# Optimization experiments

Measured on AMD Instinct MI355X. Metric: run time of the kernel, lower is better.

## Reference

```python
import jax, jax.numpy as jnp
import numpy as np
from itertools import product

G = 96          # voxel grid side
B = 2           # batch samples
N_PER = 60000   # occupied voxels per sample
N = B * N_PER
C_IN = 64
C_OUT = 1
NUM_BLOCKS = 2
EPS = 1e-5


def _build_kernel_map():
    """Emulate MinkowskiEngine's coordinate hash map for a k=3, stride=1, 3D conv.
    Returns batch_ids [N], and per-offset (in_idx, out_idx) padded to N with sentinel N."""
    rng = np.random.default_rng(0)
    side = G - 2  # coords in [1, G-2] so offset coords never wrap
    keys_list = []
    for b in range(B):
        lin = rng.choice(side ** 3, size=N_PER, replace=False)
        x = lin // (side * side) + 1
        y = (lin // side) % side + 1
        z = lin % side + 1
        keys_list.append(b * G ** 3 + x * G * G + y * G + z)
    keys = np.concatenate(keys_list)
    batch_ids = np.repeat(np.arange(B), N_PER).astype(np.int32)
    order = np.argsort(keys)
    skeys = keys[order]
    in_idx = np.full((27, N), N, np.int32)   # sentinel N -> zero-padded feature row
    out_idx = np.full((27, N), N, np.int32)  # sentinel N -> dropped output row
    for k, (dx, dy, dz) in enumerate(product((-1, 0, 1), repeat=3)):
        nk = keys + dx * G * G + dy * G + dz  # neighbor coordinate key per output voxel
        pos = np.searchsorted(skeys, nk)
        pc = np.clip(pos, 0, N - 1)
        valid = skeys[pc] == nk
        m = int(valid.sum())
        in_idx[k, :m] = order[pc[valid]]
        out_idx[k, :m] = np.nonzero(valid)[0]
    return batch_ids, in_idx, out_idx


def instance_norm(f, batch_ids, num_batches):
    # per-sample, per-channel normalization over all voxels of each sample (ME InstanceNorm, no affine)
    cnt = jax.ops.segment_sum(jnp.ones((f.shape[0],), f.dtype), batch_ids, num_segments=num_batches)
    mean = jax.ops.segment_sum(f, batch_ids, num_segments=num_batches) / cnt[:, None]
    fc = f - mean[batch_ids]
    var = jax.ops.segment_sum(fc * fc, batch_ids, num_segments=num_batches) / cnt[:, None]
    return fc * jax.lax.rsqrt(var + EPS)[batch_ids]


def sparse_conv(f, w, in_idx, out_idx, bias=None):
    # gather-matmul-scatter per kernel offset; w: [27, Cin, Cout]
    n = f.shape[0]
    fpad = jnp.concatenate([f, jnp.zeros((1, f.shape[1]), f.dtype)], axis=0)
    out = jnp.zeros((n + 1, w.shape[-1]), f.dtype)
    for k in range(w.shape[0]):  # static 27-iteration loop over kernel offsets
        out = out.at[out_idx[k]].add(fpad[in_idx[k]] @ w[k])
    out = out[:n]
    if bias is not None:
        out = out + bias
    return out


def setup_inputs() -> dict:
    batch_ids, in_idx, out_idx = _build_kernel_map()
    key = jax.random.key(0)
    k0, k1, k2, k3 = jax.random.split(key, 4)
    feats = jax.random.normal(k0, (N, C_IN), dtype=jnp.float32)
    w_blocks = jax.random.normal(k1, (NUM_BLOCKS, 2, 27, C_IN, C_IN), dtype=jnp.float32) * 0.02
    w_final = jax.random.normal(k2, (27, C_IN, C_OUT), dtype=jnp.float32) * 0.02
    b_final = jax.random.normal(k3, (C_OUT,), dtype=jnp.float32) * 0.02
    return {
        "feats": feats,
        "w_blocks": w_blocks,
        "w_final": w_final,
        "b_final": b_final,
        "in_idx": jnp.asarray(in_idx),
        "out_idx": jnp.asarray(out_idx),
        "batch_ids": jnp.asarray(batch_ids),
        "batch_size": B,
    }


def reference(feats, w_blocks, w_final, b_final, in_idx, out_idx, batch_ids, batch_size):
    # InstanceNorm + ReLU
    x = jax.nn.relu(instance_norm(feats, batch_ids, batch_size))
    # SparseBasicBlocks: conv -> IN -> relu -> conv -> IN -> +res -> relu
    for b in range(w_blocks.shape[0]):
        res = x
        h = sparse_conv(x, w_blocks[b, 0], in_idx, out_idx)
        h = jax.nn.relu(instance_norm(h, batch_ids, batch_size))
        h = sparse_conv(h, w_blocks[b, 1], in_idx, out_idx)
        h = instance_norm(h, batch_ids, batch_size)
        x = jax.nn.relu(h + res)
    # final conv with bias
    return sparse_conv(x, w_final, in_idx, out_idx, bias=b_final)
```

## Files before the change

### kernel.cpp

```cpp
#include <hip/hip_runtime.h>

#define NPTS 120000
#define NROW 120064
#define NB   60000
#define TAPS 27
#define NBLK (NROW / 128)

typedef short  short8 __attribute__((ext_vector_type(8)));
typedef float  f32x4  __attribute__((ext_vector_type(4)));

__device__ __forceinline__ float bf2f(unsigned short u) {
  unsigned v = ((unsigned)u) << 16;
  float f; __builtin_memcpy(&f, &v, 4); return f;
}
__device__ __forceinline__ unsigned short f2bf(float f) {
  unsigned v; __builtin_memcpy(&v, &f, 4);
  v = v + 0x7FFFu + ((v >> 16) & 1u);
  return (unsigned short)(v >> 16);
}

__global__ __launch_bounds__(256) void k_build_nbr(const int* __restrict__ oi,
                                                   const int* __restrict__ ii,
                                                   int* __restrict__ nbr) {
  int g = blockIdx.x * 256 + threadIdx.x;
  if (g >= TAPS * NPTS) return;
  int o = oi[g];
  if (o < NPTS) nbr[(g / NPTS) * NROW + o] = ii[g];
}

__global__ __launch_bounds__(256) void k_repack(const float* __restrict__ w,
                                                unsigned short* __restrict__ wp) {
  int g = blockIdx.x * 256 + threadIdx.x;
  int e = g & 7, l = (g >> 3) & 63, f = (g >> 9) & 7, rest = g >> 12;
  int t = f >> 1, h = f & 1;
  int kk = h * 32 + (l >> 4) * 8 + e;
  int cc = t * 16 + (l & 15);
  wp[g] = f2bf(w[(rest * 64 + kk) * 64 + cc]);
}

__global__ __launch_bounds__(256) void k_stats1_f32(const float* __restrict__ F,
                                                    float* __restrict__ SM) {
  int lane = threadIdx.x & 63, wave = threadIdx.x >> 6;
  int batch = blockIdx.x >> 7, bb = blockIdx.x & 127;
  const float* Fb = F + (size_t)batch * NB * 64;
  float s = 0.f, ss = 0.f;
  for (int r = bb * 4 + wave; r < NB; r += 512) {
    float v = Fb[(size_t)r * 64 + lane];
    s += v; ss += v * v;
  }
  __shared__ float ls[4][64], lss[4][64];
  ls[wave][lane] = s; lss[wave][lane] = ss;
  __syncthreads();
  if (threadIdx.x < 64) {
    float S  = ls[0][lane] + ls[1][lane] + ls[2][lane] + ls[3][lane];
    float SS = lss[0][lane] + lss[1][lane] + lss[2][lane] + lss[3][lane];
    atomicAdd(&SM[(batch * 2 + 0) * 64 + lane], S);
    atomicAdd(&SM[(batch * 2 + 1) * 64 + lane], SS);
  }
}

__global__ __launch_bounds__(256) void k_apply_f2b(const float* __restrict__ F,
                                                   const float* __restrict__ SM,
                                                   unsigned short* __restrict__ O) {
  int i = blockIdx.x * 256 + threadIdx.x;
  int r = i >> 3, cb = (i & 7) * 8;
  int b = (r >= NB) ? 1 : 0;
  f32x4 v0 = *((const f32x4*)F + i * 2);
  f32x4 v1 = *((const f32x4*)F + i * 2 + 1);
  short8 o;
#pragma unroll
  for (int e = 0; e < 8; ++e) {
    float mean = SM[(b * 2 + 0) * 64 + cb + e] * (1.f / NB);
    float var  = SM[(b * 2 + 1) * 64 + cb + e] * (1.f / NB) - mean * mean;
    float rstd = rsqrtf(var + 1e-5f);
    float x = (e < 4) ? v0[e & 3] : v1[e & 3];
    o[e] = (short)f2bf(fmaxf((x - mean) * rstd, 0.f));
  }
  *((short8*)O + i) = o;
}

__global__ __launch_bounds__(256) void k_apply_bf(const unsigned short* __restrict__ F,
                                                  const float* __restrict__ SM,
                                                  unsigned short* __restrict__ O) {
  int i = blockIdx.x * 256 + threadIdx.x;
  int r = i >> 3, cb = (i & 7) * 8;
  int b = (r >= NB) ? 1 : 0;
  short8 v = *((const short8*)F + i);
  short8 o;
#pragma unroll
  for (int e = 0; e < 8; ++e) {
    float mean = SM[(b * 2 + 0) * 64 + cb + e] * (1.f / NB);
    float var  = SM[(b * 2 + 1) * 64 + cb + e] * (1.f / NB) - mean * mean;
    float rstd = rsqrtf(var + 1e-5f);
    float f = (bf2f((unsigned short)v[e]) - mean) * rstd;
    o[e] = (short)f2bf(fmaxf(f, 0.f));
  }
  *((short8*)O + i) = o;
}

__global__ __launch_bounds__(256) void k_apply_res_bf(const unsigned short* __restrict__ H2,
                                                      const float* __restrict__ SM,
                                                      unsigned short* __restrict__ X) {
  int i = blockIdx.x * 256 + threadIdx.x;
  int r = i >> 3, cb = (i & 7) * 8;
  int b = (r >= NB) ? 1 : 0;
  short8 v = *((const short8*)H2 + i);
  short8 xv = *((const short8*)X + i);
  short8 o;
#pragma unroll
  for (int e = 0; e < 8; ++e) {
    float mean = SM[(b * 2 + 0) * 64 + cb + e] * (1.f / NB);
    float var  = SM[(b * 2 + 1) * 64 + cb + e] * (1.f / NB) - mean * mean;
    float rstd = rsqrtf(var + 1e-5f);
    float f = (bf2f((unsigned short)v[e]) - mean) * rstd + bf2f((unsigned short)xv[e]);
    o[e] = (short)f2bf(fmaxf(f, 0.f));
  }
  *((short8*)X + i) = o;
}

__global__ __launch_bounds__(256) void k_conv64s(const unsigned short* __restrict__ X,
                                                 const unsigned short* __restrict__ WP,
                                                 const int* __restrict__ nbr,
                                                 unsigned short* __restrict__ Y,
                                                 float* __restrict__ SM) {
  const int lane = threadIdx.x & 63, wave = threadIdx.x >> 6;
  const int j0w = blockIdx.x * 128 + wave * 32;
  const int lrow = lane & 15, lk = lane >> 4;
  const int nb0 = j0w + lrow;
  f32x4 acc[2][4];
#pragma unroll
  for (int g = 0; g < 2; ++g)
#pragma unroll
    for (int c = 0; c < 4; ++c) acc[g][c] = (f32x4){0.f, 0.f, 0.f, 0.f};

  short8 aA[2][2], aB[2][2];

  auto GATHER = [&](int k, short8 (&a)[2][2]) {
    const int* np = nbr + (size_t)k * NROW + nb0;
    int i0 = np[0], i1 = np[16];
    const unsigned short* r0 = X + (size_t)(i0 >= 0 ? i0 : NROW) * 64 + lk * 8;
    const unsigned short* r1 = X + (size_t)(i1 >= 0 ? i1 : NROW) * 64 + lk * 8;
    a[0][0] = *(const short8*)r0; a[0][1] = *(const short8*)(r0 + 32);
    a[1][0] = *(const short8*)r1; a[1][1] = *(const short8*)(r1 + 32);
  };
  auto TAP = [&](int k, short8 (&a)[2][2]) {
    const unsigned short* wpk = WP + k * 4096 + lane * 8;
#pragma unroll
    for (int ct = 0; ct < 4; ++ct) {
      short8 b0 = *(const short8*)(wpk + ct * 1024);
      short8 b1 = *(const short8*)(wpk + ct * 1024 + 512);
      acc[0][ct] = __builtin_amdgcn_mfma_f32_16x16x32_bf16(a[0][0], b0, acc[0][ct], 0, 0, 0);
      acc[0][ct] = __builtin_amdgcn_mfma_f32_16x16x32_bf16(a[0][1], b1, acc[0][ct], 0, 0, 0);
      acc[1][ct] = __builtin_amdgcn_mfma_f32_16x16x32_bf16(a[1][0], b0, acc[1][ct], 0, 0, 0);
      acc[1][ct] = __builtin_amdgcn_mfma_f32_16x16x32_bf16(a[1][1], b1, acc[1][ct], 0, 0, 0);
    }
  };

  GATHER(0, aA);
#pragma unroll
  for (int kk = 0; kk < TAPS; kk += 2) {
    if (kk + 1 < TAPS) GATHER(kk + 1, aB);
    TAP(kk, aA);
    if (kk + 1 < TAPS) {
      if (kk + 2 < TAPS) GATHER(kk + 2, aA);
      TAP(kk + 1, aB);
    }
  }

#pragma unroll
  for (int g = 0; g < 2; ++g) {
    unsigned short* yp = Y + (size_t)(j0w + g * 16 + lk * 4) * 64 + lrow;
#pragma unroll
    for (int r = 0; r < 4; ++r) {
      yp[r * 64 +  0] = f2bf(acc[g][0][r]);
      yp[r * 64 + 16] = f2bf(acc[g][1][r]);
      yp[r * 64 + 32] = f2bf(acc[g][2][r]);
      yp[r * 64 + 48] = f2bf(acc[g][3][r]);
    }
  }

  float s[4][2], q[4][2];
#pragma unroll
  for (int ct = 0; ct < 4; ++ct) { s[ct][0] = s[ct][1] = q[ct][0] = q[ct][1] = 0.f; }
#pragma unroll
  for (int g = 0; g < 2; ++g) {
    int rowbase = j0w + g * 16 + lk * 4;
#pragma unroll
    for (int r = 0; r < 4; ++r) {
      int bt = (rowbase + r) >= NB;
#pragma unroll
      for (int ct = 0; ct < 4; ++ct) {
        float v = acc[g][ct][r];
        s[ct][bt] += v; q[ct][bt] += v * v;
      }
    }
  }
  __shared__ float sred[4][4][4][64];
#pragma unroll
  for (int ct = 0; ct < 4; ++ct)
#pragma unroll
    for (int b = 0; b < 2; ++b) {
      sred[wave][lk][b * 2 + 0][ct * 16 + lrow] = s[ct][b];
      sred[wave][lk][b * 2 + 1][ct * 16 + lrow] = q[ct][b];
    }
  __syncthreads();
  int t = threadIdx.x;
  float S = 0.f;
#pragma unroll
  for (int w = 0; w < 4; ++w)
#pragma unroll
    for (int l2 = 0; l2 < 4; ++l2)
      S += sred[w][l2][t >> 6][t & 63];
  atomicAdd(&SM[t], S);
}

__global__ __launch_bounds__(256) void k_dfin(const unsigned short* __restrict__ X,
                                              const float* __restrict__ WF,
                                              float* __restrict__ D) {
  const int lane = threadIdx.x & 63, wave = threadIdx.x >> 6;
  const int j0 = blockIdx.x * 64 + wave * 16;
  const int lrow = lane & 15, lk = lane >> 4;
  const unsigned short* rp = X + (size_t)(j0 + lrow) * 64 + lk * 8;
  short8 a0 = *(const short8*)rp;
  short8 a1 = *(const short8*)(rp + 32);
  short8 b[2][2];
#pragma unroll
  for (int ct = 0; ct < 2; ++ct) {
    int col = ct * 16 + lrow;
#pragma unroll
    for (int h = 0; h < 2; ++h) {
#pragma unroll
      for (int e = 0; e < 8; ++e)
        b[ct][h][e] = (col < TAPS) ? (short)f2bf(WF[col * 64 + h * 32 + lk * 8 + e]) : (short)0;
    }
  }
  f32x4 acc0 = {0,0,0,0}, acc1 = {0,0,0,0};
  acc0 = __builtin_amdgcn_mfma_f32_16x16x32_bf16(a0, b[0][0], acc0, 0, 0, 0);
  acc0 = __builtin_amdgcn_mfma_f32_16x16x32_bf16(a1, b[0][1], acc0, 0, 0, 0);
  acc1 = __builtin_amdgcn_mfma_f32_16x16x32_bf16(a0, b[1][0], acc1, 0, 0, 0);
  acc1 = __builtin_amdgcn_mfma_f32_16x16x32_bf16(a1, b[1][1], acc1, 0, 0, 0);
  float* dp0 = D + (size_t)lrow * NROW + j0 + lk * 4;
  float* dp1 = D + (size_t)(16 + lrow) * NROW + j0 + lk * 4;
#pragma unroll
  for (int r = 0; r < 4; ++r) { dp0[r] = acc0[r]; dp1[r] = acc1[r]; }
}

__global__ __launch_bounds__(256) void k_gfin(const float* __restrict__ D,
                                              const int* __restrict__ nbr,
                                              const float* __restrict__ BF,
                                              float* __restrict__ out) {
  int j = blockIdx.x * 256 + threadIdx.x;
  if (j >= NPTS) return;
  float acc = BF[0];
#pragma unroll
  for (int k = 0; k < TAPS; ++k) {
    int idx = nbr[(size_t)k * NROW + j];
    if (idx >= 0) acc += D[(size_t)k * NROW + idx];
  }
  out[j] = acc;
}

extern "C" void kernel_launch(void* const* d_in, const int* in_sizes, int n_in,
                              void* d_out, int out_size, void* d_ws, size_t ws_size,
                              hipStream_t stream) {
  (void)in_sizes; (void)n_in; (void)out_size; (void)ws_size;
  const float* feats = (const float*)d_in[0];
  const float* wblk  = (const float*)d_in[1];
  const float* wfin  = (const float*)d_in[2];
  const float* bfin  = (const float*)d_in[3];
  const int* in_idx  = (const int*)d_in[4];
  const int* out_idx = (const int*)d_in[5];

  char* p = (char*)d_ws;
  size_t off = 0;
  auto carve = [&](size_t bytes) {
    void* r = p + off; off += (bytes + 255) & ~(size_t)255; return r;
  };
  int*            nbr = (int*)carve((size_t)TAPS * NROW * 4);
  unsigned short* Xb  = (unsigned short*)carve((size_t)(NROW + 1) * 64 * 2);
  unsigned short* Hb  = (unsigned short*)carve((size_t)(NROW + 1) * 64 * 2);
  unsigned short* H2b = (unsigned short*)carve((size_t)NROW * 64 * 2);
  unsigned short* WP  = (unsigned short*)carve(108u * 4096u * 2);
  float*          D   = (float*)carve((size_t)32 * NROW * 4);
  float*          SMa = (float*)carve(5 * 256 * 4);

  float* SM0 = SMa;
  float* SM1 = SMa + 256;
  float* SM2 = SMa + 512;
  float* SM3 = SMa + 768;
  float* SM4 = SMa + 1024;

  hipMemsetAsync(nbr, 0xFF, (size_t)TAPS * NROW * 4, stream);
  hipMemsetAsync(SMa, 0, 5 * 256 * 4, stream);
  hipMemsetAsync(Xb + (size_t)NROW * 64, 0, 128, stream);
  hipMemsetAsync(Hb + (size_t)NROW * 64, 0, 128, stream);
  k_build_nbr<<<(TAPS * NPTS + 255) / 256, 256, 0, stream>>>(out_idx, in_idx, nbr);
  k_repack<<<1728, 256, 0, stream>>>(wblk, WP);

  k_stats1_f32<<<256, 256, 0, stream>>>(feats, SM0);
  k_apply_f2b<<<3750, 256, 0, stream>>>(feats, SM0, Xb);

  k_conv64s<<<NBLK, 256, 0, stream>>>(Xb, WP + 0 * 110592, nbr, Hb, SM1);
  k_apply_bf<<<3750, 256, 0, stream>>>(Hb, SM1, Hb);
  k_conv64s<<<NBLK, 256, 0, stream>>>(Hb, WP + 1 * 110592, nbr, H2b, SM2);
  k_apply_res_bf<<<3750, 256, 0, stream>>>(H2b, SM2, Xb);

  k_conv64s<<<NBLK, 256, 0, stream>>>(Xb, WP + 2 * 110592, nbr, Hb, SM3);
  k_apply_bf<<<3750, 256, 0, stream>>>(Hb, SM3, Hb);
  k_conv64s<<<NBLK, 256, 0, stream>>>(Hb, WP + 3 * 110592, nbr, H2b, SM4);
  k_apply_res_bf<<<3750, 256, 0, stream>>>(H2b, SM4, Xb);

  k_dfin<<<NROW / 64, 256, 0, stream>>>(Xb, wfin, D);
  k_gfin<<<NROW / 256, 256, 0, stream>>>(D, nbr, bfin, (float*)d_out);
}
```

Measured before the change: 451.4 us.

## Stage conv weights in LDS with double-buffered async loads and skip empty taps

The sparse conv kernel now copies each tap's 64x64 bf16 weight slice into a double-buffered LDS area using global_load_lds, prefetching the next tap while the current one is computed. Every wave then reads weights from LDS instead of each wave reading them from global memory. Taps where no row in the wave has a valid neighbor skip the gather and the MFMAs, decided by a wave ballot. In exchange the explicit register double-buffering of gathered rows is gone, a block-wide barrier is added on every tap, and the loop is no longer unrolled, so gather latency may be hidden less well.

```diff
diff --git a/kernel.cpp b/kernel.cpp
--- a/kernel.cpp
+++ b/kernel.cpp
@@ -8,6 +8,9 @@
 
 typedef short  short8 __attribute__((ext_vector_type(8)));
 typedef float  f32x4  __attribute__((ext_vector_type(4)));
+typedef unsigned int u32;
+#define GLB __attribute__((address_space(1)))
+#define LDS __attribute__((address_space(3)))
 
 __device__ __forceinline__ float bf2f(unsigned short u) {
   unsigned v = ((unsigned)u) << 16;
@@ -124,47 +127,57 @@
                                                  unsigned short* __restrict__ Y,
                                                  float* __restrict__ SM) {
   const int lane = threadIdx.x & 63, wave = threadIdx.x >> 6;
+  const int t = threadIdx.x;
   const int j0w = blockIdx.x * 128 + wave * 32;
   const int lrow = lane & 15, lk = lane >> 4;
   const int nb0 = j0w + lrow;
+
+  __shared__ unsigned short wbuf[2][4096];
+  __shared__ float sred[4][4][4][64];
+
+  {
+    const unsigned short* g = WP;
+    __builtin_amdgcn_global_load_lds((GLB const u32*)(g + t * 8),
+                                     (LDS u32*)&wbuf[0][t * 8], 16, 0, 0);
+    __builtin_amdgcn_global_load_lds((GLB const u32*)(g + (t + 256) * 8),
+                                     (LDS u32*)&wbuf[0][(t + 256) * 8], 16, 0, 0);
+  }
+  __syncthreads();
+
   f32x4 acc[2][4];
 #pragma unroll
   for (int g = 0; g < 2; ++g)
 #pragma unroll
     for (int c = 0; c < 4; ++c) acc[g][c] = (f32x4){0.f, 0.f, 0.f, 0.f};
 
-  short8 aA[2][2], aB[2][2];
-
-  auto GATHER = [&](int k, short8 (&a)[2][2]) {
+  for (int k = 0; k < TAPS; ++k) {
+    const int cur = k & 1;
+    if (k + 1 < TAPS) {
+      const unsigned short* g = WP + (k + 1) * 4096;
+      __builtin_amdgcn_global_load_lds((GLB const u32*)(g + t * 8),
+                                       (LDS u32*)&wbuf[cur ^ 1][t * 8], 16, 0, 0);
+      __builtin_amdgcn_global_load_lds((GLB const u32*)(g + (t + 256) * 8),
+                                       (LDS u32*)&wbuf[cur ^ 1][(t + 256) * 8], 16, 0, 0);
+    }
     const int* np = nbr + (size_t)k * NROW + nb0;
     int i0 = np[0], i1 = np[16];
-    const unsigned short* r0 = X + (size_t)(i0 >= 0 ? i0 : NROW) * 64 + lk * 8;
-    const unsigned short* r1 = X + (size_t)(i1 >= 0 ? i1 : NROW) * 64 + lk * 8;
-    a[0][0] = *(const short8*)r0; a[0][1] = *(const short8*)(r0 + 32);
-    a[1][0] = *(const short8*)r1; a[1][1] = *(const short8*)(r1 + 32);
-  };
-  auto TAP = [&](int k, short8 (&a)[2][2]) {
-    const unsigned short* wpk = WP + k * 4096 + lane * 8;
-#pragma unroll
-    for (int ct = 0; ct < 4; ++ct) {
-      short8 b0 = *(const short8*)(wpk + ct * 1024);
-      short8 b1 = *(const short8*)(wpk + ct * 1024 + 512);
-      acc[0][ct] = __builtin_amdgcn_mfma_f32_16x16x32_bf16(a[0][0], b0, acc[0][ct], 0, 0, 0);
-      acc[0][ct] = __builtin_amdgcn_mfma_f32_16x16x32_bf16(a[0][1], b1, acc[0][ct], 0, 0, 0);
-      acc[1][ct] = __builtin_amdgcn_mfma_f32_16x16x32_bf16(a[1][0], b0, acc[1][ct], 0, 0, 0);
-      acc[1][ct] = __builtin_amdgcn_mfma_f32_16x16x32_bf16(a[1][1], b1, acc[1][ct], 0, 0, 0);
-    }
-  };
-
-  GATHER(0, aA);
-#pragma unroll
-  for (int kk = 0; kk < TAPS; kk += 2) {
-    if (kk + 1 < TAPS) GATHER(kk + 1, aB);
-    TAP(kk, aA);
-    if (kk + 1 < TAPS) {
-      if (kk + 2 < TAPS) GATHER(kk + 2, aA);
-      TAP(kk + 1, aB);
-    }
+    if (__ballot(i0 >= 0 || i1 >= 0) != 0ull) {
+      const unsigned short* r0 = X + (size_t)(i0 >= 0 ? i0 : NROW) * 64 + lk * 8;
+      const unsigned short* r1 = X + (size_t)(i1 >= 0 ? i1 : NROW) * 64 + lk * 8;
+      short8 a00 = *(const short8*)r0, a01 = *(const short8*)(r0 + 32);
+      short8 a10 = *(const short8*)r1, a11 = *(const short8*)(r1 + 32);
+      const unsigned short* wl = &wbuf[cur][lane * 8];
+#pragma unroll
+      for (int ct = 0; ct < 4; ++ct) {
+        short8 b0 = *(const short8*)(wl + ct * 1024);
+        short8 b1 = *(const short8*)(wl + ct * 1024 + 512);
+        acc[0][ct] = __builtin_amdgcn_mfma_f32_16x16x32_bf16(a00, b0, acc[0][ct], 0, 0, 0);
+        acc[0][ct] = __builtin_amdgcn_mfma_f32_16x16x32_bf16(a01, b1, acc[0][ct], 0, 0, 0);
+        acc[1][ct] = __builtin_amdgcn_mfma_f32_16x16x32_bf16(a10, b0, acc[1][ct], 0, 0, 0);
+        acc[1][ct] = __builtin_amdgcn_mfma_f32_16x16x32_bf16(a11, b1, acc[1][ct], 0, 0, 0);
+      }
+    }
+    __syncthreads();
   }
 
 #pragma unroll
@@ -195,7 +208,6 @@
       }
     }
   }
-  __shared__ float sred[4][4][4][64];
 #pragma unroll
   for (int ct = 0; ct < 4; ++ct)
 #pragma unroll
@@ -204,7 +216,6 @@
       sred[wave][lk][b * 2 + 1][ct * 16 + lrow] = q[ct][b];
     }
   __syncthreads();
-  int t = threadIdx.x;
   float S = 0.f;
 #pragma unroll
   for (int w = 0; w < 4; ++w)
```

New measurement: 451.4 us. About the same (-0.0%).
